# Performance work log

Measured on AMD Instinct MI355X. Metric: run time of the kernel, lower is better.

## Reference

```python
import jax, jax.numpy as jnp
import numpy as np

FP8_MAX = 448.0  # max normal of float8_e4m3fn (TE fwd format)
EPS = 1e-12


def _fp8_quant_dequant(t):
    """Per-tensor amax scaling -> cast to e4m3 -> dequant back to f32.
    Mirrors TE's per-tensor scaling recipe (scale = FP8_MAX / amax)."""
    amax = jnp.max(jnp.abs(t))
    scale = FP8_MAX / jnp.maximum(amax, EPS)
    q = jnp.clip(t * scale, -FP8_MAX, FP8_MAX).astype(jnp.float8_e4m3fn)
    return q.astype(jnp.float32) / scale


def setup_inputs() -> dict:
    key = jax.random.key(0)
    k1, k2, k3 = jax.random.split(key, 3)
    tokens, d_in, d_out = 8192, 4096, 4096
    x = jax.random.normal(k1, (tokens, d_in), dtype=jnp.float32)
    # kaiming_uniform_(a=sqrt(5)) -> U(-bound, bound), bound = sqrt(6/((1+a^2)*fan_in)) = 1/sqrt(fan_in)
    bound = 1.0 / np.sqrt(d_in)
    weight = jax.random.uniform(k2, (d_out, d_in), dtype=jnp.float32, minval=-bound, maxval=bound)
    bias = jnp.zeros((d_out,), dtype=jnp.float32) + 0.01 * jax.random.normal(k3, (d_out,), dtype=jnp.float32)
    return {"x": x, "weight": weight, "bias": bias}


def reference(x, weight, bias):
    # fp8 quant/dequant of activations and weights, then GEMM + bias
    xq = _fp8_quant_dequant(x)            # [T, Din]
    wq = _fp8_quant_dequant(weight)       # [Dout, Din]
    out = jnp.einsum("ti,oi->to", xq, wq) # [T, Dout]
    return out + bias[None, :]
```

## Files before the change

### kernel.cpp

```cpp
#include <hip/hip_runtime.h>
#include <stdint.h>

#define M_DIM 8192
#define N_DIM 4096
#define K_DIM 4096

typedef float f32x4 __attribute__((ext_vector_type(4)));
typedef int   i32x4 __attribute__((ext_vector_type(4)));
typedef int   i32x8 __attribute__((ext_vector_type(8)));

__global__ __launch_bounds__(256) void amax2_kernel(const float* __restrict__ x,
                                                    const float* __restrict__ wgt,
                                                    unsigned int* __restrict__ ws_u) {
    const int which = blockIdx.y;
    const float4* p = (const float4*)(which ? wgt : x);
    const int n4 = (which ? N_DIM : M_DIM) * (K_DIM / 4);
    int tid = blockIdx.x * blockDim.x + threadIdx.x;
    int stride = gridDim.x * blockDim.x;
    float m = 0.0f;
    for (int i = tid; i < n4; i += stride) {
        float4 v = p[i];
        m = fmaxf(m, fmaxf(fmaxf(fabsf(v.x), fabsf(v.y)),
                           fmaxf(fabsf(v.z), fabsf(v.w))));
    }
#pragma unroll
    for (int off = 32; off > 0; off >>= 1)
        m = fmaxf(m, __shfl_down(m, off, 64));
    __shared__ float sm[4];
    if ((threadIdx.x & 63) == 0) sm[threadIdx.x >> 6] = m;
    __syncthreads();
    if (threadIdx.x == 0) {
        m = fmaxf(fmaxf(sm[0], sm[1]), fmaxf(sm[2], sm[3]));
        atomicMax(ws_u + which, __float_as_uint(m));
    }
}

__global__ __launch_bounds__(256) void quant2_kernel(const float* __restrict__ x,
                                                     const float* __restrict__ wgt,
                                                     unsigned int* __restrict__ xq,
                                                     unsigned int* __restrict__ wq,
                                                     const unsigned int* __restrict__ ws_u) {
    const int which = blockIdx.y;
    const float4* p = (const float4*)(which ? wgt : x);
    unsigned int* outp = which ? wq : xq;
    const int n4 = (which ? N_DIM : M_DIM) * (K_DIM / 4);
    float amax = fmaxf(__uint_as_float(ws_u[which]), 1e-12f);
    float scale = 448.0f / amax;
    int tid = blockIdx.x * blockDim.x + threadIdx.x;
    int stride = gridDim.x * blockDim.x;
    for (int i = tid; i < n4; i += stride) {
        float4 v = p[i];
        float a = fminf(fmaxf(v.x * scale, -448.0f), 448.0f);
        float b = fminf(fmaxf(v.y * scale, -448.0f), 448.0f);
        float c = fminf(fmaxf(v.z * scale, -448.0f), 448.0f);
        float d = fminf(fmaxf(v.w * scale, -448.0f), 448.0f);
        int w = __builtin_amdgcn_cvt_pk_fp8_f32(a, b, 0, false);
        w = __builtin_amdgcn_cvt_pk_fp8_f32(c, d, w, true);
        outp[i] = (unsigned int)w;
    }
}

__device__ __forceinline__ void gld16(const void* g, void* l) {
    __builtin_amdgcn_global_load_lds(
        (const __attribute__((address_space(1))) void*)g,
        (__attribute__((address_space(3))) void*)l, 16, 0, 0);
}

#define MFMA_MX(a, b, c) __builtin_amdgcn_mfma_scale_f32_16x16x128_f8f6f4( \
    (a), (b), (c), 0, 0, 0, 0x7F7F7F7F, 0, 0x7F7F7F7F)
#define BAR()    __builtin_amdgcn_s_barrier()
#define VMCNT(n) asm volatile("s_waitcnt vmcnt(" #n ")" ::: "memory")
#define PRIO1()  __builtin_amdgcn_s_setprio(1)
#define PRIO0()  __builtin_amdgcn_s_setprio(0)

__global__ __launch_bounds__(512, 4) void gemm_fp8_kernel(
    const uint8_t* __restrict__ Aq,
    const uint8_t* __restrict__ Bq,
    const float* __restrict__ bias,
    const unsigned int* __restrict__ ws_u,
    float* __restrict__ out)
{
    __shared__ uint8_t lds[49152];

    const int tid = threadIdx.x;
    const int w = tid >> 6, l = tid & 63;

    const int cpx = (int)gridDim.x >> 3;
    const int bid = (int)blockIdx.x;
    const int swz = (bid & 7) * cpx + (bid >> 3);
    const int bm = swz >> 5, bn = swz & 31;

    const uint8_t* gA = Aq + (size_t)bm * 256 * K_DIM;
    const uint8_t* gB = Bq + (size_t)bn * 128 * K_DIM;

    const int idx = tid >> 3, p = tid & 7;
    const int srcX = ((p ^ (idx & 7)) << 4);
    const uint8_t* aRow = gA + (size_t)idx * K_DIM + srcX;
    const uint8_t* bRow = gB + (size_t)idx * K_DIM + srcX;
    const int dA = tid * 16;

    const int wr = w >> 1, wc = w & 1;
    const int lr = l & 15, g = l >> 4;
    const int oLo = (((2 * g) ^ (lr & 7)) << 4);
    const int oHi = (((2 * g + 1) ^ (lr & 7)) << 4);
    const int rowA0 = wr * 64 + lr;
    const int rowB0 = wc * 64 + lr;

    auto stage = [&](int kn) {
        gld16(aRow + kn,                          &lds[dA]);
        gld16(aRow + (size_t)64  * K_DIM + kn,    &lds[8192 + dA]);
        gld16(aRow + (size_t)128 * K_DIM + kn,    &lds[16384 + dA]);
        gld16(aRow + (size_t)192 * K_DIM + kn,    &lds[24576 + dA]);
        gld16(bRow + kn,                          &lds[32768 + dA]);
        gld16(bRow + (size_t)64  * K_DIM + kn,    &lds[40960 + dA]);
    };
    auto ldfA = [&](int row) -> i32x8 {
        const uint8_t* q = &lds[row << 7];
        i32x4 lo = *(const i32x4*)(q + oLo);
        i32x4 hi = *(const i32x4*)(q + oHi);
        return __builtin_shufflevector(lo, hi, 0, 1, 2, 3, 4, 5, 6, 7);
    };
    auto ldfB = [&](int row) -> i32x8 {
        const uint8_t* q = &lds[32768 + (row << 7)];
        i32x4 lo = *(const i32x4*)(q + oLo);
        i32x4 hi = *(const i32x4*)(q + oHi);
        return __builtin_shufflevector(lo, hi, 0, 1, 2, 3, 4, 5, 6, 7);
    };

    f32x4 acc[4][4] = {};
    i32x8 av[4], bv[2];

    stage(0);

    for (int t = 0; t < 32; ++t) {
        VMCNT(0);
        BAR();

        bv[0] = ldfB(rowB0);      bv[1] = ldfB(rowB0 + 16);
        av[0] = ldfA(rowA0);      av[1] = ldfA(rowA0 + 16);
        av[2] = ldfA(rowA0 + 32); av[3] = ldfA(rowA0 + 48);
        PRIO1();
        acc[0][0] = MFMA_MX(av[0], bv[0], acc[0][0]);
        acc[0][1] = MFMA_MX(av[0], bv[1], acc[0][1]);
        acc[1][0] = MFMA_MX(av[1], bv[0], acc[1][0]);
        acc[1][1] = MFMA_MX(av[1], bv[1], acc[1][1]);
        acc[2][0] = MFMA_MX(av[2], bv[0], acc[2][0]);
        acc[2][1] = MFMA_MX(av[2], bv[1], acc[2][1]);
        acc[3][0] = MFMA_MX(av[3], bv[0], acc[3][0]);
        acc[3][1] = MFMA_MX(av[3], bv[1], acc[3][1]);
        PRIO0();

        bv[0] = ldfB(rowB0 + 32); bv[1] = ldfB(rowB0 + 48);
        PRIO1();
        acc[0][2] = MFMA_MX(av[0], bv[0], acc[0][2]);
        acc[0][3] = MFMA_MX(av[0], bv[1], acc[0][3]);
        acc[1][2] = MFMA_MX(av[1], bv[0], acc[1][2]);
        acc[1][3] = MFMA_MX(av[1], bv[1], acc[1][3]);
        acc[2][2] = MFMA_MX(av[2], bv[0], acc[2][2]);
        acc[2][3] = MFMA_MX(av[2], bv[1], acc[2][3]);
        acc[3][2] = MFMA_MX(av[3], bv[0], acc[3][2]);
        acc[3][3] = MFMA_MX(av[3], bv[1], acc[3][3]);
        PRIO0();

        BAR();
        if (t < 31) stage((t + 1) * 128);
    }

    const float ax = fmaxf(__uint_as_float(ws_u[0]), 1e-12f);
    const float aw = fmaxf(__uint_as_float(ws_u[1]), 1e-12f);
    const float inv = (ax * (1.0f / 448.0f)) * (aw * (1.0f / 448.0f));

    const int orow0 = bm * 256 + wr * 64 + g * 4;
    const int ocol0 = bn * 128 + wc * 64 + lr;
#pragma unroll
    for (int mb = 0; mb < 4; ++mb) {
#pragma unroll
        for (int nb = 0; nb < 4; ++nb) {
            const int col = ocol0 + nb * 16;
            const float bvv = bias[col];
#pragma unroll
            for (int j = 0; j < 4; ++j) {
                const int row = orow0 + mb * 16 + j;
                out[(size_t)row * N_DIM + col] = acc[mb][nb][j] * inv + bvv;
            }
        }
    }
}

extern "C" void kernel_launch(void* const* d_in, const int* in_sizes, int n_in,
                              void* d_out, int out_size, void* d_ws, size_t ws_size,
                              hipStream_t stream) {
    const float* x    = (const float*)d_in[0];
    const float* wgt  = (const float*)d_in[1];
    const float* bias = (const float*)d_in[2];
    float* out = (float*)d_out;

    unsigned int* ws_u = (unsigned int*)d_ws;
    uint8_t* xq = (uint8_t*)d_ws + 256;
    uint8_t* wq = xq + (size_t)M_DIM * K_DIM;

    hipMemsetAsync(d_ws, 0, 8, stream);

    dim3 ga(1024, 2);
    amax2_kernel<<<ga, 256, 0, stream>>>(x, wgt, ws_u);

    dim3 gq(2048, 2);
    quant2_kernel<<<gq, 256, 0, stream>>>(x, wgt, (unsigned int*)xq,
                                          (unsigned int*)wq, ws_u);

    gemm_fp8_kernel<<<(M_DIM / 256) * (N_DIM / 128), 512, 0, stream>>>(
        xq, wq, bias, ws_u, out);
}
```

Before: 230.6 us.

## Switch GEMM to 256x256 tiles with 32x32x64 MFMA and double-buffered LDS

The FP8 GEMM moves from 256x128 tiles with 512 threads to 256x256 tiles with 256 threads. Each wave now computes a 128x128 sub-tile using 32x32x64 scaled MFMAs. LDS grows to 128KB as a double buffer, so the next K-slice is issued asynchronously while the current one is computed, and the trailing barrier is dropped. The aim is higher arithmetic intensity per byte loaded and global load latency hidden behind MFMA work. In exchange, occupancy falls to one block of four waves per CU and register pressure rises sharply (256 accumulator floats per thread), and the grid shrinks to 512 blocks.

```diff
diff --git a/kernel.cpp b/kernel.cpp
--- a/kernel.cpp
+++ b/kernel.cpp
@@ -5,9 +5,10 @@
 #define N_DIM 4096
 #define K_DIM 4096
 
-typedef float f32x4 __attribute__((ext_vector_type(4)));
-typedef int   i32x4 __attribute__((ext_vector_type(4)));
-typedef int   i32x8 __attribute__((ext_vector_type(8)));
+typedef float f32x4  __attribute__((ext_vector_type(4)));
+typedef float f32x16 __attribute__((ext_vector_type(16)));
+typedef int   i32x4  __attribute__((ext_vector_type(4)));
+typedef int   i32x8  __attribute__((ext_vector_type(8)));
 
 __global__ __launch_bounds__(256) void amax2_kernel(const float* __restrict__ x,
                                                     const float* __restrict__ wgt,
@@ -66,21 +67,22 @@
         (__attribute__((address_space(3))) void*)l, 16, 0, 0);
 }
 
-#define MFMA_MX(a, b, c) __builtin_amdgcn_mfma_scale_f32_16x16x128_f8f6f4( \
+#define MFMA32(a, b, c) __builtin_amdgcn_mfma_scale_f32_32x32x64_f8f6f4( \
     (a), (b), (c), 0, 0, 0, 0x7F7F7F7F, 0, 0x7F7F7F7F)
 #define BAR()    __builtin_amdgcn_s_barrier()
 #define VMCNT(n) asm volatile("s_waitcnt vmcnt(" #n ")" ::: "memory")
 #define PRIO1()  __builtin_amdgcn_s_setprio(1)
 #define PRIO0()  __builtin_amdgcn_s_setprio(0)
-
-__global__ __launch_bounds__(512, 4) void gemm_fp8_kernel(
+#define FENCE()  asm volatile("" ::: "memory")
+
+__global__ __launch_bounds__(256, 1) void gemm_fp8_kernel(
     const uint8_t* __restrict__ Aq,
     const uint8_t* __restrict__ Bq,
     const float* __restrict__ bias,
     const unsigned int* __restrict__ ws_u,
     float* __restrict__ out)
 {
-    __shared__ uint8_t lds[49152];
+    __shared__ uint8_t lds[131072];
 
     const int tid = threadIdx.x;
     const int w = tid >> 6, l = tid & 63;
@@ -88,10 +90,10 @@
     const int cpx = (int)gridDim.x >> 3;
     const int bid = (int)blockIdx.x;
     const int swz = (bid & 7) * cpx + (bid >> 3);
-    const int bm = swz >> 5, bn = swz & 31;
+    const int bm = swz >> 4, bn = swz & 15;
 
     const uint8_t* gA = Aq + (size_t)bm * 256 * K_DIM;
-    const uint8_t* gB = Bq + (size_t)bn * 128 * K_DIM;
+    const uint8_t* gB = Bq + (size_t)bn * 256 * K_DIM;
 
     const int idx = tid >> 3, p = tid & 7;
     const int srcX = ((p ^ (idx & 7)) << 4);
@@ -100,88 +102,121 @@
     const int dA = tid * 16;
 
     const int wr = w >> 1, wc = w & 1;
-    const int lr = l & 15, g = l >> 4;
-    const int oLo = (((2 * g) ^ (lr & 7)) << 4);
-    const int oHi = (((2 * g + 1) ^ (lr & 7)) << 4);
-    const int rowA0 = wr * 64 + lr;
-    const int rowB0 = wc * 64 + lr;
-
-    auto stage = [&](int kn) {
-        gld16(aRow + kn,                          &lds[dA]);
-        gld16(aRow + (size_t)64  * K_DIM + kn,    &lds[8192 + dA]);
-        gld16(aRow + (size_t)128 * K_DIM + kn,    &lds[16384 + dA]);
-        gld16(aRow + (size_t)192 * K_DIM + kn,    &lds[24576 + dA]);
-        gld16(bRow + kn,                          &lds[32768 + dA]);
-        gld16(bRow + (size_t)64  * K_DIM + kn,    &lds[40960 + dA]);
+    const int lr = l & 31;
+    const int hi2 = (l >> 5) << 1;
+    const int rowA0 = wr * 128 + lr;
+    const int rowB0 = wc * 128 + lr;
+
+    auto stageA = [&](int bb, int kn, int half) {
+#pragma unroll
+        for (int r = 0; r < 4; ++r)
+            gld16(aRow + (size_t)(half * 128 + r * 32) * K_DIM + kn,
+                  &lds[bb * 32768 + half * 16384 + r * 4096 + dA]);
     };
-    auto ldfA = [&](int row) -> i32x8 {
-        const uint8_t* q = &lds[row << 7];
-        i32x4 lo = *(const i32x4*)(q + oLo);
-        i32x4 hi = *(const i32x4*)(q + oHi);
-        return __builtin_shufflevector(lo, hi, 0, 1, 2, 3, 4, 5, 6, 7);
+    auto stageB = [&](int bb, int kn, int half) {
+#pragma unroll
+        for (int r = 0; r < 4; ++r)
+            gld16(bRow + (size_t)(half * 128 + r * 32) * K_DIM + kn,
+                  &lds[65536 + bb * 32768 + half * 16384 + r * 4096 + dA]);
     };
-    auto ldfB = [&](int row) -> i32x8 {
-        const uint8_t* q = &lds[32768 + (row << 7)];
-        i32x4 lo = *(const i32x4*)(q + oLo);
-        i32x4 hi = *(const i32x4*)(q + oHi);
-        return __builtin_shufflevector(lo, hi, 0, 1, 2, 3, 4, 5, 6, 7);
+    auto ldf = [&](const uint8_t* base, int row, int kh) -> i32x8 {
+        const uint8_t* q = base + (row << 7);
+        const int rk = row & 7;
+        const int c0 = (kh << 2) + hi2;
+        i32x4 lo = *(const i32x4*)(q + ((c0 ^ rk) << 4));
+        i32x4 hh = *(const i32x4*)(q + (((c0 + 1) ^ rk) << 4));
+        return __builtin_shufflevector(lo, hh, 0, 1, 2, 3, 4, 5, 6, 7);
     };
 
-    f32x4 acc[4][4] = {};
-    i32x8 av[4], bv[2];
-
-    stage(0);
+    f32x16 acc[4][4] = {};
+    i32x8 av[4], bv[4];
+
+    stageA(0, 0, 0); stageB(0, 0, 0);
+    stageA(0, 0, 1); stageB(0, 0, 1);
 
     for (int t = 0; t < 32; ++t) {
+        const int buf = t & 1, nbuf = buf ^ 1;
+        const int kn = (t + 1) * 128;
+        const uint8_t* lab = &lds[buf * 32768];
+        const uint8_t* lbb = &lds[65536 + buf * 32768];
+
         VMCNT(0);
         BAR();
 
-        bv[0] = ldfB(rowB0);      bv[1] = ldfB(rowB0 + 16);
-        av[0] = ldfA(rowA0);      av[1] = ldfA(rowA0 + 16);
-        av[2] = ldfA(rowA0 + 32); av[3] = ldfA(rowA0 + 48);
-        PRIO1();
-        acc[0][0] = MFMA_MX(av[0], bv[0], acc[0][0]);
-        acc[0][1] = MFMA_MX(av[0], bv[1], acc[0][1]);
-        acc[1][0] = MFMA_MX(av[1], bv[0], acc[1][0]);
-        acc[1][1] = MFMA_MX(av[1], bv[1], acc[1][1]);
-        acc[2][0] = MFMA_MX(av[2], bv[0], acc[2][0]);
-        acc[2][1] = MFMA_MX(av[2], bv[1], acc[2][1]);
-        acc[3][0] = MFMA_MX(av[3], bv[0], acc[3][0]);
-        acc[3][1] = MFMA_MX(av[3], bv[1], acc[3][1]);
-        PRIO0();
-
-        bv[0] = ldfB(rowB0 + 32); bv[1] = ldfB(rowB0 + 48);
-        PRIO1();
-        acc[0][2] = MFMA_MX(av[0], bv[0], acc[0][2]);
-        acc[0][3] = MFMA_MX(av[0], bv[1], acc[0][3]);
-        acc[1][2] = MFMA_MX(av[1], bv[0], acc[1][2]);
-        acc[1][3] = MFMA_MX(av[1], bv[1], acc[1][3]);
-        acc[2][2] = MFMA_MX(av[2], bv[0], acc[2][2]);
-        acc[2][3] = MFMA_MX(av[2], bv[1], acc[2][3]);
-        acc[3][2] = MFMA_MX(av[3], bv[0], acc[3][2]);
-        acc[3][3] = MFMA_MX(av[3], bv[1], acc[3][3]);
-        PRIO0();
-
-        BAR();
-        if (t < 31) stage((t + 1) * 128);
+        if (t < 31) { stageA(nbuf, kn, 0); stageB(nbuf, kn, 0); }
+        bv[0] = ldf(lbb, rowB0, 0);      bv[1] = ldf(lbb, rowB0 + 32, 0);
+        av[0] = ldf(lab, rowA0, 0);      av[1] = ldf(lab, rowA0 + 32, 0);
+        av[2] = ldf(lab, rowA0 + 64, 0); av[3] = ldf(lab, rowA0 + 96, 0);
+        PRIO1();
+        acc[0][0] = MFMA32(av[0], bv[0], acc[0][0]);
+        acc[0][1] = MFMA32(av[0], bv[1], acc[0][1]);
+        acc[1][0] = MFMA32(av[1], bv[0], acc[1][0]);
+        acc[1][1] = MFMA32(av[1], bv[1], acc[1][1]);
+        acc[2][0] = MFMA32(av[2], bv[0], acc[2][0]);
+        acc[2][1] = MFMA32(av[2], bv[1], acc[2][1]);
+        acc[3][0] = MFMA32(av[3], bv[0], acc[3][0]);
+        acc[3][1] = MFMA32(av[3], bv[1], acc[3][1]);
+        PRIO0();
+        FENCE();
+
+        if (t < 31) { stageA(nbuf, kn, 1); stageB(nbuf, kn, 1); }
+        bv[2] = ldf(lbb, rowB0 + 64, 0); bv[3] = ldf(lbb, rowB0 + 96, 0);
+        PRIO1();
+        acc[0][2] = MFMA32(av[0], bv[2], acc[0][2]);
+        acc[0][3] = MFMA32(av[0], bv[3], acc[0][3]);
+        acc[1][2] = MFMA32(av[1], bv[2], acc[1][2]);
+        acc[1][3] = MFMA32(av[1], bv[3], acc[1][3]);
+        acc[2][2] = MFMA32(av[2], bv[2], acc[2][2]);
+        acc[2][3] = MFMA32(av[2], bv[3], acc[2][3]);
+        acc[3][2] = MFMA32(av[3], bv[2], acc[3][2]);
+        acc[3][3] = MFMA32(av[3], bv[3], acc[3][3]);
+        PRIO0();
+        FENCE();
+
+        av[0] = ldf(lab, rowA0, 1);      av[1] = ldf(lab, rowA0 + 32, 1);
+        av[2] = ldf(lab, rowA0 + 64, 1); av[3] = ldf(lab, rowA0 + 96, 1);
+        bv[0] = ldf(lbb, rowB0, 1);      bv[1] = ldf(lbb, rowB0 + 32, 1);
+        PRIO1();
+        acc[0][0] = MFMA32(av[0], bv[0], acc[0][0]);
+        acc[0][1] = MFMA32(av[0], bv[1], acc[0][1]);
+        acc[1][0] = MFMA32(av[1], bv[0], acc[1][0]);
+        acc[1][1] = MFMA32(av[1], bv[1], acc[1][1]);
+        acc[2][0] = MFMA32(av[2], bv[0], acc[2][0]);
+        acc[2][1] = MFMA32(av[2], bv[1], acc[2][1]);
+        acc[3][0] = MFMA32(av[3], bv[0], acc[3][0]);
+        acc[3][1] = MFMA32(av[3], bv[1], acc[3][1]);
+        PRIO0();
+        FENCE();
+
+        bv[2] = ldf(lbb, rowB0 + 64, 1); bv[3] = ldf(lbb, rowB0 + 96, 1);
+        PRIO1();
+        acc[0][2] = MFMA32(av[0], bv[2], acc[0][2]);
+        acc[0][3] = MFMA32(av[0], bv[3], acc[0][3]);
+        acc[1][2] = MFMA32(av[1], bv[2], acc[1][2]);
+        acc[1][3] = MFMA32(av[1], bv[3], acc[1][3]);
+        acc[2][2] = MFMA32(av[2], bv[2], acc[2][2]);
+        acc[2][3] = MFMA32(av[2], bv[3], acc[2][3]);
+        acc[3][2] = MFMA32(av[3], bv[2], acc[3][2]);
+        acc[3][3] = MFMA32(av[3], bv[3], acc[3][3]);
+        PRIO0();
     }
 
     const float ax = fmaxf(__uint_as_float(ws_u[0]), 1e-12f);
     const float aw = fmaxf(__uint_as_float(ws_u[1]), 1e-12f);
     const float inv = (ax * (1.0f / 448.0f)) * (aw * (1.0f / 448.0f));
 
-    const int orow0 = bm * 256 + wr * 64 + g * 4;
-    const int ocol0 = bn * 128 + wc * 64 + lr;
+    const int orow0 = bm * 256 + wr * 128 + ((l >> 5) << 2);
+    const int ocol0 = bn * 256 + wc * 128 + lr;
 #pragma unroll
     for (int mb = 0; mb < 4; ++mb) {
 #pragma unroll
         for (int nb = 0; nb < 4; ++nb) {
-            const int col = ocol0 + nb * 16;
+            const int col = ocol0 + nb * 32;
             const float bvv = bias[col];
 #pragma unroll
-            for (int j = 0; j < 4; ++j) {
-                const int row = orow0 + mb * 16 + j;
-                out[(size_t)row * N_DIM + col] = acc[mb][nb][j] * inv + bvv;
+            for (int r = 0; r < 16; ++r) {
+                const int row = orow0 + mb * 32 + (r & 3) + ((r >> 2) << 3);
+                out[(size_t)row * N_DIM + col] = acc[mb][nb][r] * inv + bvv;
             }
         }
     }
@@ -208,6 +243,6 @@
     quant2_kernel<<<gq, 256, 0, stream>>>(x, wgt, (unsigned int*)xq,
                                           (unsigned int*)wq, ws_u);
 
-    gemm_fp8_kernel<<<(M_DIM / 256) * (N_DIM / 128), 512, 0, stream>>>(
+    gemm_fp8_kernel<<<(M_DIM / 256) * (N_DIM / 256), 256, 0, stream>>>(
         xq, wq, bias, ws_u, out);
 }
```

New measurement: 215.8 us. 6.4% less time.
